# Kernel tuning notes

Hardware: AMD Instinct MI355X
Metric: run time of the kernel (lower is better)

The kernel has to match this reference:

```python
import math
import jax, jax.numpy as jnp
import numpy as np

B, T, C, HS = 4, 4096, 1024, 64  # batch, seq, n_embd, head_size=n_embd//n_head

def setup_inputs() -> dict:
    key = jax.random.key(0)
    k0, k1, k2, k3 = jax.random.split(key, 4)
    x = jax.random.normal(k0, (B, T, C), dtype=jnp.float32)
    Wq = jax.random.normal(k1, (C, HS), dtype=jnp.float32) * 0.02
    Wk = jax.random.normal(k2, (C, HS), dtype=jnp.float32) * 0.02
    Wv = jax.random.normal(k3, (C, HS), dtype=jnp.float32) * 0.02
    return {"x": x, "Wq": Wq, "Wk": Wk, "Wv": Wv}

def reference(x, Wq, Wk, Wv):
    b, t, c = x.shape
    q = x @ Wq                                   # [B,T,hs]
    k = x @ Wk                                   # [B,T,hs]
    v = x @ Wv                                   # [B,T,hs]
    wei = jnp.einsum('btd,bsd->bts', q, k)       # [B,T,T] raw scores
    row_sums = wei.sum(axis=-1)                  # [B,T]
    k_sel = math.ceil(t / 2)                     # static: t known at trace time
    _, idx = jax.lax.top_k(row_sums, k_sel)      # [B,k_sel]
    idx = jnp.sort(idx, axis=1)
    # gather selected score rows: [B,k_sel,T]
    half_wei = jnp.take_along_axis(wei, idx[:, :, None], axis=1)
    # causal mask rows gathered from tril: tril[idx[b,i], j] == (j <= idx[b,i])
    half_mask = jnp.arange(t)[None, None, :] <= idx[:, :, None]  # [B,k_sel,T] bool
    half_wei = half_wei * (c ** -0.5)            # NOTE: scaled by n_embd, as in source
    half_wei = jnp.where(half_mask, half_wei, -jnp.inf)
    att = jax.nn.softmax(half_wei, axis=-1)      # [B,k_sel,T]
    out = att @ v                                # [B,k_sel,hs]
    return out
```

## Files before the change

kernel.cpp:

```cpp
#include <hip/hip_runtime.h>
#include <math.h>

#define BB 4
#define TT 4096
#define CC 1024
#define HS 64
#define KSEL 2048
#define NSPL 16
#define SWLOG 8
#define SW 256

typedef float f32x4 __attribute__((ext_vector_type(4)));
typedef short short8 __attribute__((ext_vector_type(8)));

__device__ __forceinline__ unsigned short f2bf(float f) {
  union { float f; unsigned int u; } c;
  c.f = f;
  const unsigned int u = c.u;
  return (unsigned short)((u + 0x7FFFu + ((u >> 16) & 1u)) >> 16);
}

__device__ __forceinline__ unsigned cvtpk(float lo, float hi) {
  unsigned r;
  asm("v_cvt_pk_bf16_f32 %0, %1, %2" : "=v"(r) : "v"(lo), "v"(hi));
  return r;
}

__global__ __launch_bounds__(256) void conv_w(const float* __restrict__ Wq,
                                              const float* __restrict__ Wk,
                                              const float* __restrict__ Wv,
                                              unsigned short* __restrict__ wbf,
                                              float* __restrict__ xsum) {
  const int gid = blockIdx.x * 256 + threadIdx.x;
  if (gid < 1024)
    ((float4*)xsum)[gid] = make_float4(0.f, 0.f, 0.f, 0.f);
  const int kt = gid / 768;
  const int rem = gid - kt * 768;
  const int nt = rem >> 6, lane = rem & 63;
  const int col = nt * 16 + (lane & 15);
  const float* W = (col < 64) ? Wq : ((col < 128) ? Wk : Wv);
  const int cl = col & 63;
  const int k0 = kt * 32 + (lane >> 4) * 8;
  unsigned short tmp[8];
#pragma unroll
  for (int i = 0; i < 8; i++) tmp[i] = f2bf(W[(size_t)(k0 + i) * HS + cl]);
  uint4 o;
  o.x = tmp[0] | ((unsigned)tmp[1] << 16);
  o.y = tmp[2] | ((unsigned)tmp[3] << 16);
  o.z = tmp[4] | ((unsigned)tmp[5] << 16);
  o.w = tmp[6] | ((unsigned)tmp[7] << 16);
  *(uint4*)(wbf + (size_t)gid * 8) = o;
}

#define PR 16
__global__ __launch_bounds__(256) void fusedproj(
    const float* __restrict__ x, const unsigned short* __restrict__ wbf,
    float* __restrict__ xsum, unsigned short* __restrict__ qbf,
    unsigned short* __restrict__ kbf, unsigned short* __restrict__ vtbf) {
  __shared__ unsigned short Xs[2][PR][256];
  __shared__ float xsred[2][4][256];
  const int rb = blockIdx.x;
  const size_t r0 = (size_t)rb * PR;
  const int tid = threadIdx.x;
  const int wid = tid >> 6, lane = tid & 63;
  const int lhi = lane >> 4, llo = lane & 15;
  const int cl = tid & 63, rg = tid >> 6;
  const int bidx = rb >> 8;

  f32x4 acc[3];
#pragma unroll
  for (int n = 0; n < 3; n++) acc[n] = (f32x4){0.f, 0.f, 0.f, 0.f};

  float4 pf[4];
#pragma unroll
  for (int rr = 0; rr < 4; rr++)
    pf[rr] = *(const float4*)(x + (r0 + rg * 4 + rr) * CC + cl * 4);

  {
    float ps0 = 0.f, ps1 = 0.f, ps2 = 0.f, ps3 = 0.f;
#pragma unroll
    for (int rr = 0; rr < 4; rr++) {
      const int row = rg * 4 + rr;
      float4 v = pf[rr];
      ps0 += v.x; ps1 += v.y; ps2 += v.z; ps3 += v.w;
      *(uint2*)((char*)&Xs[0][0][0] + row * 512 +
                ((((cl >> 1) ^ (row & 7))) << 4) + ((cl & 1) << 3)) =
          make_uint2(cvtpk(v.x, v.y), cvtpk(v.z, v.w));
    }
    xsred[0][rg][cl * 4 + 0] = ps0;
    xsred[0][rg][cl * 4 + 1] = ps1;
    xsred[0][rg][cl * 4 + 2] = ps2;
    xsred[0][rg][cl * 4 + 3] = ps3;
  }
  __syncthreads();

  for (int ch = 0; ch < 4; ch++) {
    const int cur = ch & 1;
    if (ch < 3) {
#pragma unroll
      for (int rr = 0; rr < 4; rr++)
        pf[rr] = *(const float4*)(x + (r0 + rg * 4 + rr) * CC +
                                  (ch + 1) * 256 + cl * 4);
    }
    atomicAdd(&xsum[bidx * CC + ch * 256 + tid],
              xsred[cur][0][tid] + xsred[cur][1][tid] + xsred[cur][2][tid] +
                  xsred[cur][3][tid]);
#pragma unroll
    for (int ktl = 0; ktl < 8; ktl++) {
      short8 af = *(const short8*)((const char*)&Xs[cur][0][0] + llo * 512 +
                                   ((((ktl << 2) + lhi) ^ (llo & 7)) << 4));
      const unsigned short* bp =
          wbf + (((size_t)(ch * 8 + ktl) * 12 + wid * 3) * 64 + lane) * 8;
#pragma unroll
      for (int n = 0; n < 3; n++) {
        short8 bf = *(const short8*)(bp + n * 64 * 8);
        acc[n] = __builtin_amdgcn_mfma_f32_16x16x32_bf16(af, bf, acc[n], 0, 0, 0);
      }
    }
    if (ch < 3) {
      float ps0 = 0.f, ps1 = 0.f, ps2 = 0.f, ps3 = 0.f;
#pragma unroll
      for (int rr = 0; rr < 4; rr++) {
        const int row = rg * 4 + rr;
        float4 v = pf[rr];
        ps0 += v.x; ps1 += v.y; ps2 += v.z; ps3 += v.w;
        *(uint2*)((char*)&Xs[cur ^ 1][0][0] + row * 512 +
                  ((((cl >> 1) ^ (row & 7))) << 4) + ((cl & 1) << 3)) =
            make_uint2(cvtpk(v.x, v.y), cvtpk(v.z, v.w));
      }
      xsred[cur ^ 1][rg][cl * 4 + 0] = ps0;
      xsred[cur ^ 1][rg][cl * 4 + 1] = ps1;
      xsred[cur ^ 1][rg][cl * 4 + 2] = ps2;
      xsred[cur ^ 1][rg][cl * 4 + 3] = ps3;
      __syncthreads();
    }
  }
  const int rbg = (int)r0 + lhi * 4;
#pragma unroll
  for (int n = 0; n < 3; n++) {
    const int col = (wid * 3 + n) * 16 + llo;
    const int mat = col >> 6, cl2 = col & 63;
    if (mat == 0) {
#pragma unroll
      for (int r = 0; r < 4; r++)
        qbf[(size_t)(rbg + r) * HS + cl2] = f2bf(acc[n][r] * 0.03125f);
    } else if (mat == 1) {
#pragma unroll
      for (int r = 0; r < 4; r++)
        kbf[(size_t)(rbg + r) * HS + cl2] = f2bf(acc[n][r]);
    } else {
      const int bb = rbg >> 12, tloc = rbg & (TT - 1);
      *(uint2*)(vtbf + ((size_t)bb * HS + cl2) * TT + tloc) =
          make_uint2(cvtpk(acc[n][0], acc[n][1]), cvtpk(acc[n][2], acc[n][3]));
    }
  }
}

__global__ __launch_bounds__(512) void rowsums_x(
    const float* __restrict__ x, const float* __restrict__ Wq,
    const float* __restrict__ Wk, const float* __restrict__ xsum,
    float* __restrict__ rs) {
  __shared__ float xsl[CC];
  __shared__ float kred[8][HS];
  __shared__ float ksl[HS];
  __shared__ float wl[CC];
  const int g = blockIdx.x;
  const int tid = threadIdx.x;
  const int b = g >> 6;
  *(float2*)(xsl + tid * 2) = *(const float2*)(xsum + b * CC + tid * 2);
  __syncthreads();
  {
    const int g8 = tid >> 6, d = tid & 63;
    const float* wkp = Wk + (size_t)(g8 * 128) * HS + d;
    float s = 0.f;
    for (int c = 0; c < 128; c++) s += xsl[g8 * 128 + c] * wkp[(size_t)c * HS];
    kred[g8][d] = s;
  }
  __syncthreads();
  if (tid < 64) {
    float s = 0.f;
#pragma unroll
    for (int g8 = 0; g8 < 8; g8++) s += kred[g8][tid];
    ksl[tid] = s;
  }
  __syncthreads();
#pragma unroll
  for (int p = 0; p < 2; p++) {
    const int c = tid * 2 + p;
    const float* wqp = Wq + (size_t)c * HS;
    float s = 0.f;
#pragma unroll
    for (int d4 = 0; d4 < 16; d4++) {
      float4 a = *(const float4*)(wqp + d4 * 4);
      float4 kk = *(const float4*)(ksl + d4 * 4);
      s += a.x * kk.x + a.y * kk.y + a.z * kk.z + a.w * kk.w;
    }
    wl[c] = s;
  }
  __syncthreads();
  const size_t row = (size_t)g * 64 + (tid >> 3);
  const int qu = tid & 7;
  const float* xr = x + row * CC + qu * 128;
  const float* wr = wl + qu * 128;
  float s = 0.f;
  for (int e = 0; e < 32; e++) {
    float4 v = *(const float4*)(xr + e * 4);
    float4 w4 = *(const float4*)(wr + e * 4);
    s += v.x * w4.x + v.y * w4.y + v.z * w4.z + v.w * w4.w;
  }
  s += __shfl_xor(s, 1);
  s += __shfl_xor(s, 2);
  s += __shfl_xor(s, 4);
  if (qu == 0) rs[row] = s;
}

__global__ __launch_bounds__(256) void rankk(const float* __restrict__ rs,
                                             int* __restrict__ flag) {
  __shared__ float rl[TT];
  const int g = blockIdx.x;
  const int b = g >> 7, chunk = g & 127;
  const int tid = threadIdx.x;
  const float* rsb = rs + (size_t)b * TT;
  for (int e = tid; e < TT / 4; e += 256)
    *(float4*)(rl + e * 4) = *(const float4*)(rsb + e * 4);
  __syncthreads();
  const int cand = tid >> 3, qu = tid & 7;
  const int t = chunk * 32 + cand;
  const float my = rl[t];
  int cnt = 0;
  for (int e = 0; e < 128; e++) {
    const int s = qu * 512 + e * 4;
    float4 v = *(const float4*)(rl + s);
    cnt += (v.x > my) || (v.x == my && (s + 0) < t);
    cnt += (v.y > my) || (v.y == my && (s + 1) < t);
    cnt += (v.z > my) || (v.z == my && (s + 2) < t);
    cnt += (v.w > my) || (v.w == my && (s + 3) < t);
  }
  cnt += __shfl_xor(cnt, 1);
  cnt += __shfl_xor(cnt, 2);
  cnt += __shfl_xor(cnt, 4);
  if (qu == 0) flag[(size_t)b * TT + t] = (cnt < KSEL) ? 1 : 0;
}

__global__ __launch_bounds__(256) void compact(const int* __restrict__ flag,
                                               int* __restrict__ idx) {
  __shared__ int wsum[4];
  __shared__ int woff[4];
  const int b = blockIdx.x;
  const int tid = threadIdx.x;
  const int wid = tid >> 6, lane = tid & 63;
  const int* fb = flag + (size_t)b * TT;
  const int base = tid * 16;
  int f[16];
  int cnt = 0;
#pragma unroll
  for (int e4 = 0; e4 < 4; e4++) {
    int4 v = *(const int4*)(fb + base + e4 * 4);
    f[e4 * 4 + 0] = v.x; f[e4 * 4 + 1] = v.y;
    f[e4 * 4 + 2] = v.z; f[e4 * 4 + 3] = v.w;
    cnt += v.x + v.y + v.z + v.w;
  }
  int sc = cnt;
#pragma unroll
  for (int d = 1; d < 64; d <<= 1) {
    int v = __shfl_up(sc, d);
    if (lane >= d) sc += v;
  }
  if (lane == 63) wsum[wid] = sc;
  __syncthreads();
  if (tid == 0) {
    int a = 0;
#pragma unroll
    for (int w = 0; w < 4; w++) { woff[w] = a; a += wsum[w]; }
  }
  __syncthreads();
  int pos = woff[wid] + sc - cnt;
#pragma unroll
  for (int e = 0; e < 16; e++)
    if (f[e]) idx[(size_t)b * KSEL + (pos++)] = base + e;
}

struct KF { short8 a0, a1, b0, b1; };
struct VF { short8 v0, v1, v2, v3; };

__global__ __launch_bounds__(256) void attn_mfma(
    const unsigned short* __restrict__ qbf,
    const unsigned short* __restrict__ kbf,
    const unsigned short* __restrict__ vtbf, const int* __restrict__ idx,
    float* __restrict__ pl, float* __restrict__ pacc) {
  __shared__ unsigned short P_lds[4][32][40];
  const int rb = blockIdx.x;
  const int zz = blockIdx.y;
  const int b = blockIdx.z;
  const int tid = threadIdx.x;
  const int wid = tid >> 6, lane = tid & 63;
  const int s = zz * 4 + wid;
  const size_t rbase = (size_t)b * KSEL + rb * 32;
  const int tmaxblk = idx[rbase + 31];
  const int jlo = s << SWLOG;
  if (jlo > tmaxblk) return;

  const int lhi = lane >> 4, llo = lane & 15;
  const int trow0 = idx[rbase + llo];
  const int trow1 = idx[rbase + 16 + llo];
  short8 qf[2][2];
  {
    const unsigned short* qp0 = qbf + ((size_t)b * TT + trow0) * HS + lhi * 8;
    const unsigned short* qp1 = qbf + ((size_t)b * TT + trow1) * HS + lhi * 8;
    qf[0][0] = *(const short8*)(qp0);
    qf[0][1] = *(const short8*)(qp0 + 32);
    qf[1][0] = *(const short8*)(qp1);
    qf[1][1] = *(const short8*)(qp1 + 32);
  }
  f32x4 o[2][4];
#pragma unroll
  for (int mtt = 0; mtt < 2; mtt++)
#pragma unroll
    for (int n = 0; n < 4; n++) o[mtt][n] = (f32x4){0.f, 0.f, 0.f, 0.f};
  float lsum[2] = {0.f, 0.f};

  const unsigned short* kb = kbf + (size_t)b * TT * HS;
  const unsigned short* vb = vtbf + (size_t)b * HS * TT;
  const int jend = min(tmaxblk + 1, jlo + SW);

  auto loadK = [&](int j0) {
    KF K;
    const unsigned short* kp = kb + (size_t)(j0 + llo) * HS + lhi * 8;
    K.a0 = *(const short8*)(kp);
    K.a1 = *(const short8*)(kp + 32);
    K.b0 = *(const short8*)(kp + 16 * HS);
    K.b1 = *(const short8*)(kp + 16 * HS + 32);
    return K;
  };
  auto loadV = [&](int j0) {
    VF V;
    const unsigned short* vp = vb + (size_t)llo * TT + j0 + lhi * 8;
    V.v0 = *(const short8*)(vp);
    V.v1 = *(const short8*)(vp + 16 * TT);
    V.v2 = *(const short8*)(vp + 32 * TT);
    V.v3 = *(const short8*)(vp + 48 * TT);
    return V;
  };

  auto body = [&](int j0, const KF& K, const VF& V) {
    f32x4 sc[2][2];
#pragma unroll
    for (int mtt = 0; mtt < 2; mtt++) {
      f32x4 a = (f32x4){0.f, 0.f, 0.f, 0.f};
      a = __builtin_amdgcn_mfma_f32_16x16x32_bf16(K.a0, qf[mtt][0], a, 0, 0, 0);
      a = __builtin_amdgcn_mfma_f32_16x16x32_bf16(K.a1, qf[mtt][1], a, 0, 0, 0);
      sc[mtt][0] = a;
      f32x4 c = (f32x4){0.f, 0.f, 0.f, 0.f};
      c = __builtin_amdgcn_mfma_f32_16x16x32_bf16(K.b0, qf[mtt][0], c, 0, 0, 0);
      c = __builtin_amdgcn_mfma_f32_16x16x32_bf16(K.b1, qf[mtt][1], c, 0, 0, 0);
      sc[mtt][1] = c;
    }
#pragma unroll
    for (int mtt = 0; mtt < 2; mtt++) {
      const int tr = (mtt == 0) ? trow0 : trow1;
      float p[8];
#pragma unroll
      for (int kt = 0; kt < 2; kt++)
#pragma unroll
        for (int r = 0; r < 4; r++) {
          const int kk = j0 + kt * 16 + lhi * 4 + r;
          const float e = __expf(sc[mtt][kt][r]);
          p[kt * 4 + r] = (kk <= tr) ? e : 0.f;
        }
      lsum[mtt] += ((p[0] + p[1]) + (p[2] + p[3])) +
                   ((p[4] + p[5]) + (p[6] + p[7]));
      *(uint2*)&P_lds[wid][mtt * 16 + llo][lhi * 4] =
          make_uint2(cvtpk(p[0], p[1]), cvtpk(p[2], p[3]));
      *(uint2*)&P_lds[wid][mtt * 16 + llo][16 + lhi * 4] =
          make_uint2(cvtpk(p[4], p[5]), cvtpk(p[6], p[7]));
    }
    short8 pa0 = *(const short8*)&P_lds[wid][llo][lhi * 8];
    short8 pa1 = *(const short8*)&P_lds[wid][16 + llo][lhi * 8];
    o[0][0] = __builtin_amdgcn_mfma_f32_16x16x32_bf16(pa0, V.v0, o[0][0], 0, 0, 0);
    o[1][0] = __builtin_amdgcn_mfma_f32_16x16x32_bf16(pa1, V.v0, o[1][0], 0, 0, 0);
    o[0][1] = __builtin_amdgcn_mfma_f32_16x16x32_bf16(pa0, V.v1, o[0][1], 0, 0, 0);
    o[1][1] = __builtin_amdgcn_mfma_f32_16x16x32_bf16(pa1, V.v1, o[1][1], 0, 0, 0);
    o[0][2] = __builtin_amdgcn_mfma_f32_16x16x32_bf16(pa0, V.v2, o[0][2], 0, 0, 0);
    o[1][2] = __builtin_amdgcn_mfma_f32_16x16x32_bf16(pa1, V.v2, o[1][2], 0, 0, 0);
    o[0][3] = __builtin_amdgcn_mfma_f32_16x16x32_bf16(pa0, V.v3, o[0][3], 0, 0, 0);
    o[1][3] = __builtin_amdgcn_mfma_f32_16x16x32_bf16(pa1, V.v3, o[1][3], 0, 0, 0);
  };

  int j0 = jlo;
  KF ka = loadK(j0), kb2;
  VF va = loadV(j0), vb2;
  for (;;) {
    if (j0 + 32 < jend) { kb2 = loadK(j0 + 32); vb2 = loadV(j0 + 32); }
    body(j0, ka, va);
    j0 += 32;
    if (j0 >= jend) break;
    if (j0 + 32 < jend) { ka = loadK(j0 + 32); va = loadV(j0 + 32); }
    body(j0, kb2, vb2);
    j0 += 32;
    if (j0 >= jend) break;
  }

  lsum[0] += __shfl_xor(lsum[0], 16);
  lsum[0] += __shfl_xor(lsum[0], 32);
  lsum[1] += __shfl_xor(lsum[1], 16);
  lsum[1] += __shfl_xor(lsum[1], 32);
  if (lane < 16) {
    pl[(rbase + llo) * NSPL + s] = lsum[0];
    pl[(rbase + 16 + llo) * NSPL + s] = lsum[1];
  }
#pragma unroll
  for (int mtt = 0; mtt < 2; mtt++)
#pragma unroll
    for (int r = 0; r < 4; r++) {
      const size_t rowi = rbase + mtt * 16 + lhi * 4 + r;
#pragma unroll
      for (int n = 0; n < 4; n++)
        pacc[(rowi * NSPL + s) * HS + n * 16 + llo] = o[mtt][n][r];
    }
}

__global__ __launch_bounds__(256) void attn_combine(
    const float* __restrict__ pl, const float* __restrict__ pacc,
    const int* __restrict__ idx, float* __restrict__ out) {
  const int b = blockIdx.x;
  const int i0 = blockIdx.y * 32;
  const int tid = threadIdx.x;
  const int r = tid >> 3, dg = tid & 7;
  const size_t rowi = (size_t)b * KSEL + i0 + r;
  const int t_r = idx[rowi];
  const int ns = (t_r >> SWLOG) + 1;
  float L = 0.f;
  float o[8] = {0.f, 0.f, 0.f, 0.f, 0.f, 0.f, 0.f, 0.f};
  for (int s = 0; s < ns; s++) {
    L += pl[rowi * NSPL + s];
    const float* pa = pacc + (rowi * NSPL + s) * HS + dg * 8;
    float4 a0 = *(const float4*)(pa);
    float4 a1 = *(const float4*)(pa + 4);
    o[0] += a0.x; o[1] += a0.y; o[2] += a0.z; o[3] += a0.w;
    o[4] += a1.x; o[5] += a1.y; o[6] += a1.z; o[7] += a1.w;
  }
  const float invl = 1.0f / L;
  float* op = out + rowi * HS + dg * 8;
  *(float4*)(op) = make_float4(o[0] * invl, o[1] * invl, o[2] * invl, o[3] * invl);
  *(float4*)(op + 4) = make_float4(o[4] * invl, o[5] * invl, o[6] * invl, o[7] * invl);
}

extern "C" void kernel_launch(void* const* d_in, const int* in_sizes, int n_in,
                              void* d_out, int out_size, void* d_ws,
                              size_t ws_size, hipStream_t stream) {
  const float* x = (const float*)d_in[0];
  const float* Wq = (const float*)d_in[1];
  const float* Wk = (const float*)d_in[2];
  const float* Wv = (const float*)d_in[3];
  float* out = (float*)d_out;

  float* wsf = (float*)d_ws;
  float* pacc = wsf;
  float* xsum = wsf;
  float* rs = xsum + 4096;
  int* flag = (int*)(rs + 16384);
  unsigned short* wbf = (unsigned short*)(flag + 16384);
  unsigned short* qbf = (unsigned short*)(pacc + 8388608);
  unsigned short* kbf = qbf + 1048576;
  unsigned short* vtbf = kbf + 1048576;
  int* idxp = (int*)(vtbf + 1048576);
  float* pl = (float*)(idxp + 8192);

  conv_w<<<96, 256, 0, stream>>>(Wq, Wk, Wv, wbf, xsum);
  fusedproj<<<1024, 256, 0, stream>>>(x, wbf, xsum, qbf, kbf, vtbf);
  rowsums_x<<<256, 512, 0, stream>>>(x, Wq, Wk, xsum, rs);
  rankk<<<512, 256, 0, stream>>>(rs, flag);
  compact<<<BB, 256, 0, stream>>>(flag, idxp);
  attn_mfma<<<dim3(64, 4, BB), 256, 0, stream>>>(qbf, kbf, vtbf, idxp, pl, pacc);
  attn_combine<<<dim3(BB, 64), 256, 0, stream>>>(pl, pacc, idxp, out);
}
```

Measured before the change: 136.0 us.

## Fuse all stages into one cooperative persistent kernel with grid syncs

Replaces the seven-kernel pipeline with a single cooperative kernel of 256 blocks that runs weight conversion, projection, row sums, ranking, compaction, split attention and combine, separated by grid.sync barriers. Work is remapped so each persistent block loops over several tiles per stage, and the projection tile grows to 32 rows with six accumulators per wave. The goal is to remove the launch gaps between kernels. The cost is that only 256 blocks run, which lowers parallelism and occupancy in the heavy projection and attention stages, and each barrier adds grid-wide sync latency. The previous multi-kernel path is kept as a fallback if the cooperative launch fails, and the fallback projection drops its LDS double buffering.

```diff
diff --git a/kernel.cpp b/kernel.cpp
--- a/kernel.cpp
+++ b/kernel.cpp
@@ -1,5 +1,8 @@
 #include <hip/hip_runtime.h>
+#include <hip/hip_cooperative_groups.h>
 #include <math.h>
+
+namespace cg = cooperative_groups;
 
 #define BB 4
 #define TT 4096
@@ -9,6 +12,7 @@
 #define NSPL 16
 #define SWLOG 8
 #define SW 256
+#define NBLK 256
 
 typedef float f32x4 __attribute__((ext_vector_type(4)));
 typedef short short8 __attribute__((ext_vector_type(8)));
@@ -26,14 +30,415 @@
   return r;
 }
 
-__global__ __launch_bounds__(256) void conv_w(const float* __restrict__ Wq,
-                                              const float* __restrict__ Wk,
-                                              const float* __restrict__ Wv,
-                                              unsigned short* __restrict__ wbf,
-                                              float* __restrict__ xsum) {
+__global__ __launch_bounds__(256) void mega(
+    const float* __restrict__ x, const float* __restrict__ Wq,
+    const float* __restrict__ Wk, const float* __restrict__ Wv,
+    float* __restrict__ out, float* __restrict__ xsum, float* __restrict__ rs,
+    int* __restrict__ flag, unsigned short* __restrict__ wbf,
+    unsigned short* __restrict__ qbf, unsigned short* __restrict__ kbf,
+    unsigned short* __restrict__ vtbf, int* __restrict__ idxp,
+    float* __restrict__ pl, float* __restrict__ pacc) {
+  __shared__ __align__(16) unsigned char SM[20480];
+  cg::grid_group grid = cg::this_grid();
+  const int blk = blockIdx.x;
+  const int tid = threadIdx.x;
+  const int wid = tid >> 6, lane = tid & 63;
+  const int lhi = lane >> 4, llo = lane & 15;
+
+  {
+    const int gid = blk * 256 + tid;
+    if (gid < 1024) ((float4*)xsum)[gid] = make_float4(0.f, 0.f, 0.f, 0.f);
+    if (gid < 24576) {
+      const int kt = gid / 768;
+      const int rem = gid - kt * 768;
+      const int nt = rem >> 6, ln = rem & 63;
+      const int col = nt * 16 + (ln & 15);
+      const float* W = (col < 64) ? Wq : ((col < 128) ? Wk : Wv);
+      const int cl = col & 63;
+      const int k0 = kt * 32 + (ln >> 4) * 8;
+      unsigned short tmp[8];
+#pragma unroll
+      for (int i = 0; i < 8; i++) tmp[i] = f2bf(W[(size_t)(k0 + i) * HS + cl]);
+      uint4 o;
+      o.x = tmp[0] | ((unsigned)tmp[1] << 16);
+      o.y = tmp[2] | ((unsigned)tmp[3] << 16);
+      o.z = tmp[4] | ((unsigned)tmp[5] << 16);
+      o.w = tmp[6] | ((unsigned)tmp[7] << 16);
+      *(uint4*)(wbf + (size_t)gid * 8) = o;
+    }
+  }
+  __threadfence();
+  grid.sync();
+
+  {
+    unsigned short* Xs = (unsigned short*)SM;
+    float* xsred = (float*)(SM + 16384);
+    const int cl = tid & 63, rg = tid >> 6;
+    const int mt = wid >> 1, nh = wid & 1;
+#pragma unroll 1
+    for (int it = 0; it < 2; ++it) {
+      const int rblk = blk * 2 + it;
+      const size_t r0 = (size_t)rblk * 32;
+      const int bidx = rblk >> 7;
+      f32x4 acc[6];
+#pragma unroll
+      for (int n = 0; n < 6; n++) acc[n] = (f32x4){0.f, 0.f, 0.f, 0.f};
+      float4 pf[8];
+#pragma unroll
+      for (int rr = 0; rr < 8; rr++)
+        pf[rr] = *(const float4*)(x + (r0 + rg * 8 + rr) * CC + cl * 4);
+
+      for (int ch = 0; ch < 4; ch++) {
+        float ps0 = 0.f, ps1 = 0.f, ps2 = 0.f, ps3 = 0.f;
+#pragma unroll
+        for (int rr = 0; rr < 8; rr++) {
+          const int row = rg * 8 + rr;
+          float4 v = pf[rr];
+          ps0 += v.x; ps1 += v.y; ps2 += v.z; ps3 += v.w;
+          *(uint2*)((char*)Xs + row * 512 + ((((cl >> 1) ^ (row & 7))) << 4) +
+                    ((cl & 1) << 3)) =
+              make_uint2(cvtpk(v.x, v.y), cvtpk(v.z, v.w));
+        }
+        xsred[rg * 256 + cl * 4 + 0] = ps0;
+        xsred[rg * 256 + cl * 4 + 1] = ps1;
+        xsred[rg * 256 + cl * 4 + 2] = ps2;
+        xsred[rg * 256 + cl * 4 + 3] = ps3;
+        __syncthreads();
+        if (ch < 3) {
+#pragma unroll
+          for (int rr = 0; rr < 8; rr++)
+            pf[rr] = *(const float4*)(x + (r0 + rg * 8 + rr) * CC +
+                                      (ch + 1) * 256 + cl * 4);
+        }
+        atomicAdd(&xsum[bidx * CC + ch * 256 + tid],
+                  xsred[tid] + xsred[256 + tid] + xsred[512 + tid] +
+                      xsred[768 + tid]);
+        const int row = mt * 16 + llo;
+#pragma unroll
+        for (int ktl = 0; ktl < 8; ktl++) {
+          short8 af =
+              *(const short8*)((const char*)Xs + row * 512 +
+                               ((((ktl << 2) + lhi) ^ (row & 7)) << 4));
+          const unsigned short* bp =
+              wbf + (((size_t)(ch * 8 + ktl) * 12 + nh * 6) * 64 + lane) * 8;
+#pragma unroll
+          for (int n = 0; n < 6; n++) {
+            short8 bf = *(const short8*)(bp + n * 64 * 8);
+            acc[n] = __builtin_amdgcn_mfma_f32_16x16x32_bf16(af, bf, acc[n],
+                                                             0, 0, 0);
+          }
+        }
+        __syncthreads();
+      }
+      const int rbg = (int)r0 + mt * 16 + lhi * 4;
+#pragma unroll
+      for (int n = 0; n < 6; n++) {
+        const int col = (nh * 6 + n) * 16 + llo;
+        const int mat = col >> 6, cl2 = col & 63;
+        if (mat == 0) {
+#pragma unroll
+          for (int r = 0; r < 4; r++)
+            qbf[(size_t)(rbg + r) * HS + cl2] = f2bf(acc[n][r] * 0.03125f);
+        } else if (mat == 1) {
+#pragma unroll
+          for (int r = 0; r < 4; r++)
+            kbf[(size_t)(rbg + r) * HS + cl2] = f2bf(acc[n][r]);
+        } else {
+          const int bb = rbg >> 12, tloc = rbg & (TT - 1);
+          *(uint2*)(vtbf + ((size_t)bb * HS + cl2) * TT + tloc) = make_uint2(
+              cvtpk(acc[n][0], acc[n][1]), cvtpk(acc[n][2], acc[n][3]));
+        }
+      }
+      __syncthreads();
+    }
+  }
+  __threadfence();
+  grid.sync();
+
+  {
+    float* xsl = (float*)SM;
+    float* kred = xsl + 1024;
+    float* ksl = kred + 256;
+    float* wl = ksl + 64;
+    const int g0 = blk * 2;
+    const int b = g0 >> 7;
+    *(float4*)(xsl + tid * 4) = *(const float4*)(xsum + b * CC + tid * 4);
+    __syncthreads();
+    {
+      float s = 0.f;
+      const float* wkp = Wk + (size_t)(wid * 256) * HS + lane;
+      for (int c = 0; c < 256; c++)
+        s += xsl[wid * 256 + c] * wkp[(size_t)c * HS];
+      kred[wid * 64 + lane] = s;
+    }
+    __syncthreads();
+    if (tid < 64)
+      ksl[tid] = kred[tid] + kred[64 + tid] + kred[128 + tid] + kred[192 + tid];
+    __syncthreads();
+#pragma unroll
+    for (int p = 0; p < 4; p++) {
+      const int c = p * 256 + tid;
+      const float* wqp = Wq + (size_t)c * HS;
+      float s = 0.f;
+#pragma unroll
+      for (int d4 = 0; d4 < 16; d4++) {
+        float4 a = *(const float4*)(wqp + d4 * 4);
+        float4 kk = *(const float4*)(ksl + d4 * 4);
+        s += a.x * kk.x + a.y * kk.y + a.z * kk.z + a.w * kk.w;
+      }
+      wl[c] = s;
+    }
+    __syncthreads();
+#pragma unroll 1
+    for (int it = 0; it < 2; ++it) {
+      const size_t row = (size_t)(g0 + it) * 32 + (tid >> 3);
+      const int qu = tid & 7;
+      const float* xr = x + row * CC + qu * 128;
+      const float* wr = wl + qu * 128;
+      float s = 0.f;
+      for (int e = 0; e < 32; e++) {
+        float4 v = *(const float4*)(xr + e * 4);
+        float4 w4 = *(const float4*)(wr + e * 4);
+        s += v.x * w4.x + v.y * w4.y + v.z * w4.z + v.w * w4.w;
+      }
+      s += __shfl_xor(s, 1);
+      s += __shfl_xor(s, 2);
+      s += __shfl_xor(s, 4);
+      if (qu == 0) rs[row] = s;
+    }
+  }
+  __threadfence();
+  grid.sync();
+
+  {
+    float* rl = (float*)SM;
+    const int g0 = blk * 2;
+    const int b = g0 >> 7;
+    const float* rsb = rs + (size_t)b * TT;
+    for (int e = tid; e < TT / 4; e += 256)
+      *(float4*)(rl + e * 4) = *(const float4*)(rsb + e * 4);
+    __syncthreads();
+#pragma unroll 1
+    for (int it = 0; it < 2; ++it) {
+      const int chunk = (g0 + it) & 127;
+      const int cand = tid >> 3, qu = tid & 7;
+      const int t = chunk * 32 + cand;
+      const float my = rl[t];
+      int cnt = 0;
+      for (int e = 0; e < 128; e++) {
+        const int s = qu * 512 + e * 4;
+        float4 v = *(const float4*)(rl + s);
+        cnt += (v.x > my) || (v.x == my && (s + 0) < t);
+        cnt += (v.y > my) || (v.y == my && (s + 1) < t);
+        cnt += (v.z > my) || (v.z == my && (s + 2) < t);
+        cnt += (v.w > my) || (v.w == my && (s + 3) < t);
+      }
+      cnt += __shfl_xor(cnt, 1);
+      cnt += __shfl_xor(cnt, 2);
+      cnt += __shfl_xor(cnt, 4);
+      if (qu == 0) flag[(size_t)b * TT + t] = (cnt < KSEL) ? 1 : 0;
+    }
+  }
+  __threadfence();
+  grid.sync();
+
+  if (blk < BB) {
+    int* wsum = (int*)SM;
+    int* woff = wsum + 4;
+    const int* fb = flag + (size_t)blk * TT;
+    const int base = tid * 16;
+    int f[16];
+    int cnt = 0;
+#pragma unroll
+    for (int e4 = 0; e4 < 4; e4++) {
+      int4 v = *(const int4*)(fb + base + e4 * 4);
+      f[e4 * 4 + 0] = v.x; f[e4 * 4 + 1] = v.y;
+      f[e4 * 4 + 2] = v.z; f[e4 * 4 + 3] = v.w;
+      cnt += v.x + v.y + v.z + v.w;
+    }
+    int sc = cnt;
+#pragma unroll
+    for (int d = 1; d < 64; d <<= 1) {
+      int v = __shfl_up(sc, d);
+      if (lane >= d) sc += v;
+    }
+    if (lane == 63) wsum[wid] = sc;
+    __syncthreads();
+    if (tid == 0) {
+      int a = 0;
+#pragma unroll
+      for (int w = 0; w < 4; w++) { woff[w] = a; a += wsum[w]; }
+    }
+    __syncthreads();
+    int pos = woff[wid] + sc - cnt;
+#pragma unroll
+    for (int e = 0; e < 16; e++)
+      if (f[e]) idxp[(size_t)blk * KSEL + (pos++)] = base + e;
+  }
+  __threadfence();
+  grid.sync();
+
+  {
+    unsigned short* P = (unsigned short*)SM;
+    unsigned short* Pw = P + wid * 32 * 40;
+#pragma unroll 1
+    for (int half = 0; half < 4; half++) {
+      const int u = (blk * 4 + wid) + half * 1024;
+      const int b = u & 3;
+      const int rb = (u >> 2) & 63;
+      const int sp = u >> 8;
+      const size_t rbase = (size_t)b * KSEL + rb * 32;
+      const int tmaxblk = idxp[rbase + 31];
+      const int jlo = sp << SWLOG;
+      if (jlo > tmaxblk) continue;
+
+      const int trow0 = idxp[rbase + llo];
+      const int trow1 = idxp[rbase + 16 + llo];
+      short8 qf[2][2];
+      {
+        const unsigned short* qp0 =
+            qbf + ((size_t)b * TT + trow0) * HS + lhi * 8;
+        const unsigned short* qp1 =
+            qbf + ((size_t)b * TT + trow1) * HS + lhi * 8;
+        qf[0][0] = *(const short8*)(qp0);
+        qf[0][1] = *(const short8*)(qp0 + 32);
+        qf[1][0] = *(const short8*)(qp1);
+        qf[1][1] = *(const short8*)(qp1 + 32);
+      }
+      f32x4 o[2][4];
+#pragma unroll
+      for (int mtt = 0; mtt < 2; mtt++)
+#pragma unroll
+        for (int n = 0; n < 4; n++) o[mtt][n] = (f32x4){0.f, 0.f, 0.f, 0.f};
+      float lsum[2] = {0.f, 0.f};
+
+      const unsigned short* kb = kbf + (size_t)b * TT * HS;
+      const unsigned short* vb = vtbf + (size_t)b * HS * TT;
+      const int jend = min(tmaxblk + 1, jlo + SW);
+
+      auto loadK = [&](int j0, short8* K) {
+        const unsigned short* kp = kb + (size_t)(j0 + llo) * HS + lhi * 8;
+        K[0] = *(const short8*)(kp);
+        K[1] = *(const short8*)(kp + 32);
+        K[2] = *(const short8*)(kp + 16 * HS);
+        K[3] = *(const short8*)(kp + 16 * HS + 32);
+      };
+      auto loadV = [&](int j0, short8* V) {
+        const unsigned short* vp = vb + (size_t)llo * TT + j0 + lhi * 8;
+        V[0] = *(const short8*)(vp);
+        V[1] = *(const short8*)(vp + 16 * TT);
+        V[2] = *(const short8*)(vp + 32 * TT);
+        V[3] = *(const short8*)(vp + 48 * TT);
+      };
+
+      auto body = [&](int j0, const short8* K, const short8* V) {
+        f32x4 sc[2][2];
+#pragma unroll
+        for (int mtt = 0; mtt < 2; mtt++) {
+          f32x4 a = (f32x4){0.f, 0.f, 0.f, 0.f};
+          a = __builtin_amdgcn_mfma_f32_16x16x32_bf16(K[0], qf[mtt][0], a, 0, 0, 0);
+          a = __builtin_amdgcn_mfma_f32_16x16x32_bf16(K[1], qf[mtt][1], a, 0, 0, 0);
+          sc[mtt][0] = a;
+          f32x4 c = (f32x4){0.f, 0.f, 0.f, 0.f};
+          c = __builtin_amdgcn_mfma_f32_16x16x32_bf16(K[2], qf[mtt][0], c, 0, 0, 0);
+          c = __builtin_amdgcn_mfma_f32_16x16x32_bf16(K[3], qf[mtt][1], c, 0, 0, 0);
+          sc[mtt][1] = c;
+        }
+#pragma unroll
+        for (int mtt = 0; mtt < 2; mtt++) {
+          const int tr = (mtt == 0) ? trow0 : trow1;
+          float p[8];
+#pragma unroll
+          for (int kt = 0; kt < 2; kt++)
+#pragma unroll
+            for (int r = 0; r < 4; r++) {
+              const int kk = j0 + kt * 16 + lhi * 4 + r;
+              const float e = __expf(sc[mtt][kt][r]);
+              p[kt * 4 + r] = (kk <= tr) ? e : 0.f;
+            }
+          lsum[mtt] += ((p[0] + p[1]) + (p[2] + p[3])) +
+                       ((p[4] + p[5]) + (p[6] + p[7]));
+          *(uint2*)&Pw[(mtt * 16 + llo) * 40 + lhi * 4] =
+              make_uint2(cvtpk(p[0], p[1]), cvtpk(p[2], p[3]));
+          *(uint2*)&Pw[(mtt * 16 + llo) * 40 + 16 + lhi * 4] =
+              make_uint2(cvtpk(p[4], p[5]), cvtpk(p[6], p[7]));
+        }
+        short8 pa0 = *(const short8*)&Pw[llo * 40 + lhi * 8];
+        short8 pa1 = *(const short8*)&Pw[(16 + llo) * 40 + lhi * 8];
+        o[0][0] = __builtin_amdgcn_mfma_f32_16x16x32_bf16(pa0, V[0], o[0][0], 0, 0, 0);
+        o[1][0] = __builtin_amdgcn_mfma_f32_16x16x32_bf16(pa1, V[0], o[1][0], 0, 0, 0);
+        o[0][1] = __builtin_amdgcn_mfma_f32_16x16x32_bf16(pa0, V[1], o[0][1], 0, 0, 0);
+        o[1][1] = __builtin_amdgcn_mfma_f32_16x16x32_bf16(pa1, V[1], o[1][1], 0, 0, 0);
+        o[0][2] = __builtin_amdgcn_mfma_f32_16x16x32_bf16(pa0, V[2], o[0][2], 0, 0, 0);
+        o[1][2] = __builtin_amdgcn_mfma_f32_16x16x32_bf16(pa1, V[2], o[1][2], 0, 0, 0);
+        o[0][3] = __builtin_amdgcn_mfma_f32_16x16x32_bf16(pa0, V[3], o[0][3], 0, 0, 0);
+        o[1][3] = __builtin_amdgcn_mfma_f32_16x16x32_bf16(pa1, V[3], o[1][3], 0, 0, 0);
+      };
+
+      int j0 = jlo;
+      short8 ka[4], kb2[4], va[4], vb2[4];
+      loadK(j0, ka);
+      loadV(j0, va);
+      for (;;) {
+        if (j0 + 32 < jend) { loadK(j0 + 32, kb2); loadV(j0 + 32, vb2); }
+        body(j0, ka, va);
+        j0 += 32;
+        if (j0 >= jend) break;
+        if (j0 + 32 < jend) { loadK(j0 + 32, ka); loadV(j0 + 32, va); }
+        body(j0, kb2, vb2);
+        j0 += 32;
+        if (j0 >= jend) break;
+      }
+
+      lsum[0] += __shfl_xor(lsum[0], 16);
+      lsum[0] += __shfl_xor(lsum[0], 32);
+      lsum[1] += __shfl_xor(lsum[1], 16);
+      lsum[1] += __shfl_xor(lsum[1], 32);
+      if (lane < 16) {
+        pl[(rbase + llo) * NSPL + sp] = lsum[0];
+        pl[(rbase + 16 + llo) * NSPL + sp] = lsum[1];
+      }
+#pragma unroll
+      for (int mtt = 0; mtt < 2; mtt++)
+#pragma unroll
+        for (int r = 0; r < 4; r++) {
+          const size_t rowi = rbase + mtt * 16 + lhi * 4 + r;
+#pragma unroll
+          for (int n = 0; n < 4; n++)
+            pacc[(rowi * NSPL + sp) * HS + n * 16 + llo] = o[mtt][n][r];
+        }
+    }
+  }
+  __threadfence();
+  grid.sync();
+
+  {
+#pragma unroll 1
+    for (int it = 0; it < 2; ++it) {
+      const int r = tid >> 4, dg = tid & 15;
+      const size_t rowi = (size_t)(blk * 2 + it) * 16 + r;
+      const int t_r = idxp[rowi];
+      const int ns = (t_r >> SWLOG) + 1;
+      float L = 0.f;
+      float o0 = 0.f, o1 = 0.f, o2 = 0.f, o3 = 0.f;
+      for (int s = 0; s < ns; s++) {
+        L += pl[rowi * NSPL + s];
+        float4 a = *(const float4*)(pacc + (rowi * NSPL + s) * HS + dg * 4);
+        o0 += a.x; o1 += a.y; o2 += a.z; o3 += a.w;
+      }
+      const float invl = 1.0f / L;
+      *(float4*)(out + rowi * HS + dg * 4) =
+          make_float4(o0 * invl, o1 * invl, o2 * invl, o3 * invl);
+    }
+  }
+}
+
+__global__ __launch_bounds__(256) void conv_w_fb(
+    const float* __restrict__ Wq, const float* __restrict__ Wk,
+    const float* __restrict__ Wv, unsigned short* __restrict__ wbf,
+    float* __restrict__ xsum) {
   const int gid = blockIdx.x * 256 + threadIdx.x;
-  if (gid < 1024)
-    ((float4*)xsum)[gid] = make_float4(0.f, 0.f, 0.f, 0.f);
+  if (gid < 1024) ((float4*)xsum)[gid] = make_float4(0.f, 0.f, 0.f, 0.f);
   const int kt = gid / 768;
   const int rem = gid - kt * 768;
   const int nt = rem >> 6, lane = rem & 63;
@@ -52,50 +457,42 @@
   *(uint4*)(wbf + (size_t)gid * 8) = o;
 }
 
-#define PR 16
-__global__ __launch_bounds__(256) void fusedproj(
+__global__ __launch_bounds__(256) void fusedproj_fb(
     const float* __restrict__ x, const unsigned short* __restrict__ wbf,
     float* __restrict__ xsum, unsigned short* __restrict__ qbf,
     unsigned short* __restrict__ kbf, unsigned short* __restrict__ vtbf) {
-  __shared__ unsigned short Xs[2][PR][256];
-  __shared__ float xsred[2][4][256];
+  __shared__ unsigned short Xs[16][256];
+  __shared__ float xsred[4][256];
   const int rb = blockIdx.x;
-  const size_t r0 = (size_t)rb * PR;
+  const size_t r0 = (size_t)rb * 16;
   const int tid = threadIdx.x;
   const int wid = tid >> 6, lane = tid & 63;
   const int lhi = lane >> 4, llo = lane & 15;
   const int cl = tid & 63, rg = tid >> 6;
   const int bidx = rb >> 8;
-
   f32x4 acc[3];
 #pragma unroll
   for (int n = 0; n < 3; n++) acc[n] = (f32x4){0.f, 0.f, 0.f, 0.f};
-
   float4 pf[4];
 #pragma unroll
   for (int rr = 0; rr < 4; rr++)
     pf[rr] = *(const float4*)(x + (r0 + rg * 4 + rr) * CC + cl * 4);
-
-  {
+  for (int ch = 0; ch < 4; ch++) {
     float ps0 = 0.f, ps1 = 0.f, ps2 = 0.f, ps3 = 0.f;
 #pragma unroll
     for (int rr = 0; rr < 4; rr++) {
       const int row = rg * 4 + rr;
       float4 v = pf[rr];
       ps0 += v.x; ps1 += v.y; ps2 += v.z; ps3 += v.w;
-      *(uint2*)((char*)&Xs[0][0][0] + row * 512 +
+      *(uint2*)((char*)&Xs[0][0] + row * 512 +
                 ((((cl >> 1) ^ (row & 7))) << 4) + ((cl & 1) << 3)) =
           make_uint2(cvtpk(v.x, v.y), cvtpk(v.z, v.w));
     }
-    xsred[0][rg][cl * 4 + 0] = ps0;
-    xsred[0][rg][cl * 4 + 1] = ps1;
-    xsred[0][rg][cl * 4 + 2] = ps2;
-    xsred[0][rg][cl * 4 + 3] = ps3;
-  }
-  __syncthreads();
-
-  for (int ch = 0; ch < 4; ch++) {
-    const int cur = ch & 1;
+    xsred[rg][cl * 4 + 0] = ps0;
+    xsred[rg][cl * 4 + 1] = ps1;
+    xsred[rg][cl * 4 + 2] = ps2;
+    xsred[rg][cl * 4 + 3] = ps3;
+    __syncthreads();
     if (ch < 3) {
 #pragma unroll
       for (int rr = 0; rr < 4; rr++)
@@ -103,11 +500,10 @@
                                   (ch + 1) * 256 + cl * 4);
     }
     atomicAdd(&xsum[bidx * CC + ch * 256 + tid],
-              xsred[cur][0][tid] + xsred[cur][1][tid] + xsred[cur][2][tid] +
-                  xsred[cur][3][tid]);
+              xsred[0][tid] + xsred[1][tid] + xsred[2][tid] + xsred[3][tid]);
 #pragma unroll
     for (int ktl = 0; ktl < 8; ktl++) {
-      short8 af = *(const short8*)((const char*)&Xs[cur][0][0] + llo * 512 +
+      short8 af = *(const short8*)((const char*)&Xs[0][0] + llo * 512 +
                                    ((((ktl << 2) + lhi) ^ (llo & 7)) << 4));
       const unsigned short* bp =
           wbf + (((size_t)(ch * 8 + ktl) * 12 + wid * 3) * 64 + lane) * 8;
@@ -117,23 +513,7 @@
         acc[n] = __builtin_amdgcn_mfma_f32_16x16x32_bf16(af, bf, acc[n], 0, 0, 0);
       }
     }
-    if (ch < 3) {
-      float ps0 = 0.f, ps1 = 0.f, ps2 = 0.f, ps3 = 0.f;
-#pragma unroll
-      for (int rr = 0; rr < 4; rr++) {
-        const int row = rg * 4 + rr;
-        float4 v = pf[rr];
-        ps0 += v.x; ps1 += v.y; ps2 += v.z; ps3 += v.w;
-        *(uint2*)((char*)&Xs[cur ^ 1][0][0] + row * 512 +
-                  ((((cl >> 1) ^ (row & 7))) << 4) + ((cl & 1) << 3)) =
-            make_uint2(cvtpk(v.x, v.y), cvtpk(v.z, v.w));
-      }
-      xsred[cur ^ 1][rg][cl * 4 + 0] = ps0;
-      xsred[cur ^ 1][rg][cl * 4 + 1] = ps1;
-      xsred[cur ^ 1][rg][cl * 4 + 2] = ps2;
-      xsred[cur ^ 1][rg][cl * 4 + 3] = ps3;
-      __syncthreads();
-    }
+    __syncthreads();
   }
   const int rbg = (int)r0 + lhi * 4;
 #pragma unroll
@@ -156,7 +536,7 @@
   }
 }
 
-__global__ __launch_bounds__(512) void rowsums_x(
+__global__ __launch_bounds__(512) void rowsums_fb(
     const float* __restrict__ x, const float* __restrict__ Wq,
     const float* __restrict__ Wk, const float* __restrict__ xsum,
     float* __restrict__ rs) {
@@ -214,8 +594,8 @@
   if (qu == 0) rs[row] = s;
 }
 
-__global__ __launch_bounds__(256) void rankk(const float* __restrict__ rs,
-                                             int* __restrict__ flag) {
+__global__ __launch_bounds__(256) void rankk_fb(const float* __restrict__ rs,
+                                                int* __restrict__ flag) {
   __shared__ float rl[TT];
   const int g = blockIdx.x;
   const int b = g >> 7, chunk = g & 127;
@@ -242,8 +622,8 @@
   if (qu == 0) flag[(size_t)b * TT + t] = (cnt < KSEL) ? 1 : 0;
 }
 
-__global__ __launch_bounds__(256) void compact(const int* __restrict__ flag,
-                                               int* __restrict__ idx) {
+__global__ __launch_bounds__(256) void compact_fb(const int* __restrict__ flag,
+                                                  int* __restrict__ idx) {
   __shared__ int wsum[4];
   __shared__ int woff[4];
   const int b = blockIdx.x;
@@ -280,10 +660,7 @@
     if (f[e]) idx[(size_t)b * KSEL + (pos++)] = base + e;
 }
 
-struct KF { short8 a0, a1, b0, b1; };
-struct VF { short8 v0, v1, v2, v3; };
-
-__global__ __launch_bounds__(256) void attn_mfma(
+__global__ __launch_bounds__(256) void attn_fb(
     const unsigned short* __restrict__ qbf,
     const unsigned short* __restrict__ kbf,
     const unsigned short* __restrict__ vtbf, const int* __restrict__ idx,
@@ -299,7 +676,6 @@
   const int tmaxblk = idx[rbase + 31];
   const int jlo = s << SWLOG;
   if (jlo > tmaxblk) return;
-
   const int lhi = lane >> 4, llo = lane & 15;
   const int trow0 = idx[rbase + llo];
   const int trow1 = idx[rbase + 16 + llo];
@@ -318,41 +694,34 @@
 #pragma unroll
     for (int n = 0; n < 4; n++) o[mtt][n] = (f32x4){0.f, 0.f, 0.f, 0.f};
   float lsum[2] = {0.f, 0.f};
-
   const unsigned short* kb = kbf + (size_t)b * TT * HS;
   const unsigned short* vb = vtbf + (size_t)b * HS * TT;
   const int jend = min(tmaxblk + 1, jlo + SW);
-
-  auto loadK = [&](int j0) {
-    KF K;
+  auto loadK = [&](int j0, short8* K) {
     const unsigned short* kp = kb + (size_t)(j0 + llo) * HS + lhi * 8;
-    K.a0 = *(const short8*)(kp);
-    K.a1 = *(const short8*)(kp + 32);
-    K.b0 = *(const short8*)(kp + 16 * HS);
-    K.b1 = *(const short8*)(kp + 16 * HS + 32);
-    return K;
+    K[0] = *(const short8*)(kp);
+    K[1] = *(const short8*)(kp + 32);
+    K[2] = *(const short8*)(kp + 16 * HS);
+    K[3] = *(const short8*)(kp + 16 * HS + 32);
   };
-  auto loadV = [&](int j0) {
-    VF V;
+  auto loadV = [&](int j0, short8* V) {
     const unsigned short* vp = vb + (size_t)llo * TT + j0 + lhi * 8;
-    V.v0 = *(const short8*)(vp);
-    V.v1 = *(const short8*)(vp + 16 * TT);
-    V.v2 = *(const short8*)(vp + 32 * TT);
-    V.v3 = *(const short8*)(vp + 48 * TT);
-    return V;
+    V[0] = *(const short8*)(vp);
+    V[1] = *(const short8*)(vp + 16 * TT);
+    V[2] = *(const short8*)(vp + 32 * TT);
+    V[3] = *(const short8*)(vp + 48 * TT);
   };
-
-  auto body = [&](int j0, const KF& K, const VF& V) {
+  auto body = [&](int j0, const short8* K, const short8* V) {
     f32x4 sc[2][2];
 #pragma unroll
     for (int mtt = 0; mtt < 2; mtt++) {
       f32x4 a = (f32x4){0.f, 0.f, 0.f, 0.f};
-      a = __builtin_amdgcn_mfma_f32_16x16x32_bf16(K.a0, qf[mtt][0], a, 0, 0, 0);
-      a = __builtin_amdgcn_mfma_f32_16x16x32_bf16(K.a1, qf[mtt][1], a, 0, 0, 0);
+      a = __builtin_amdgcn_mfma_f32_16x16x32_bf16(K[0], qf[mtt][0], a, 0, 0, 0);
+      a = __builtin_amdgcn_mfma_f32_16x16x32_bf16(K[1], qf[mtt][1], a, 0, 0, 0);
       sc[mtt][0] = a;
       f32x4 c = (f32x4){0.f, 0.f, 0.f, 0.f};
-      c = __builtin_amdgcn_mfma_f32_16x16x32_bf16(K.b0, qf[mtt][0], c, 0, 0, 0);
-      c = __builtin_amdgcn_mfma_f32_16x16x32_bf16(K.b1, qf[mtt][1], c, 0, 0, 0);
+      c = __builtin_amdgcn_mfma_f32_16x16x32_bf16(K[2], qf[mtt][0], c, 0, 0, 0);
+      c = __builtin_amdgcn_mfma_f32_16x16x32_bf16(K[3], qf[mtt][1], c, 0, 0, 0);
       sc[mtt][1] = c;
     }
 #pragma unroll
@@ -376,30 +745,29 @@
     }
     short8 pa0 = *(const short8*)&P_lds[wid][llo][lhi * 8];
     short8 pa1 = *(const short8*)&P_lds[wid][16 + llo][lhi * 8];
-    o[0][0] = __builtin_amdgcn_mfma_f32_16x16x32_bf16(pa0, V.v0, o[0][0], 0, 0, 0);
-    o[1][0] = __builtin_amdgcn_mfma_f32_16x16x32_bf16(pa1, V.v0, o[1][0], 0, 0, 0);
-    o[0][1] = __builtin_amdgcn_mfma_f32_16x16x32_bf16(pa0, V.v1, o[0][1], 0, 0, 0);
-    o[1][1] = __builtin_amdgcn_mfma_f32_16x16x32_bf16(pa1, V.v1, o[1][1], 0, 0, 0);
-    o[0][2] = __builtin_amdgcn_mfma_f32_16x16x32_bf16(pa0, V.v2, o[0][2], 0, 0, 0);
-    o[1][2] = __builtin_amdgcn_mfma_f32_16x16x32_bf16(pa1, V.v2, o[1][2], 0, 0, 0);
-    o[0][3] = __builtin_amdgcn_mfma_f32_16x16x32_bf16(pa0, V.v3, o[0][3], 0, 0, 0);
-    o[1][3] = __builtin_amdgcn_mfma_f32_16x16x32_bf16(pa1, V.v3, o[1][3], 0, 0, 0);
+    o[0][0] = __builtin_amdgcn_mfma_f32_16x16x32_bf16(pa0, V[0], o[0][0], 0, 0, 0);
+    o[1][0] = __builtin_amdgcn_mfma_f32_16x16x32_bf16(pa1, V[0], o[1][0], 0, 0, 0);
+    o[0][1] = __builtin_amdgcn_mfma_f32_16x16x32_bf16(pa0, V[1], o[0][1], 0, 0, 0);
+    o[1][1] = __builtin_amdgcn_mfma_f32_16x16x32_bf16(pa1, V[1], o[1][1], 0, 0, 0);
+    o[0][2] = __builtin_amdgcn_mfma_f32_16x16x32_bf16(pa0, V[2], o[0][2], 0, 0, 0);
+    o[1][2] = __builtin_amdgcn_mfma_f32_16x16x32_bf16(pa1, V[2], o[1][2], 0, 0, 0);
+    o[0][3] = __builtin_amdgcn_mfma_f32_16x16x32_bf16(pa0, V[3], o[0][3], 0, 0, 0);
+    o[1][3] = __builtin_amdgcn_mfma_f32_16x16x32_bf16(pa1, V[3], o[1][3], 0, 0, 0);
   };
-
   int j0 = jlo;
-  KF ka = loadK(j0), kb2;
-  VF va = loadV(j0), vb2;
+  short8 ka[4], kb2[4], va[4], vb2[4];
+  loadK(j0, ka);
+  loadV(j0, va);
   for (;;) {
-    if (j0 + 32 < jend) { kb2 = loadK(j0 + 32); vb2 = loadV(j0 + 32); }
+    if (j0 + 32 < jend) { loadK(j0 + 32, kb2); loadV(j0 + 32, vb2); }
     body(j0, ka, va);
     j0 += 32;
     if (j0 >= jend) break;
-    if (j0 + 32 < jend) { ka = loadK(j0 + 32); va = loadV(j0 + 32); }
+    if (j0 + 32 < jend) { loadK(j0 + 32, ka); loadV(j0 + 32, va); }
     body(j0, kb2, vb2);
     j0 += 32;
     if (j0 >= jend) break;
   }
-
   lsum[0] += __shfl_xor(lsum[0], 16);
   lsum[0] += __shfl_xor(lsum[0], 32);
   lsum[1] += __shfl_xor(lsum[1], 16);
@@ -419,7 +787,7 @@
     }
 }
 
-__global__ __launch_bounds__(256) void attn_combine(
+__global__ __launch_bounds__(256) void combine_fb(
     const float* __restrict__ pl, const float* __restrict__ pacc,
     const int* __restrict__ idx, float* __restrict__ out) {
   const int b = blockIdx.x;
@@ -466,11 +834,20 @@
   int* idxp = (int*)(vtbf + 1048576);
   float* pl = (float*)(idxp + 8192);
 
-  conv_w<<<96, 256, 0, stream>>>(Wq, Wk, Wv, wbf, xsum);
-  fusedproj<<<1024, 256, 0, stream>>>(x, wbf, xsum, qbf, kbf, vtbf);
-  rowsums_x<<<256, 512, 0, stream>>>(x, Wq, Wk, xsum, rs);
-  rankk<<<512, 256, 0, stream>>>(rs, flag);
-  compact<<<BB, 256, 0, stream>>>(flag, idxp);
-  attn_mfma<<<dim3(64, 4, BB), 256, 0, stream>>>(qbf, kbf, vtbf, idxp, pl, pacc);
-  attn_combine<<<dim3(BB, 64), 256, 0, stream>>>(pl, pacc, idxp, out);
-}
+  void* args[] = {(void*)&x,    (void*)&Wq,   (void*)&Wk,   (void*)&Wv,
+                  (void*)&out,  (void*)&xsum, (void*)&rs,   (void*)&flag,
+                  (void*)&wbf,  (void*)&qbf,  (void*)&kbf,  (void*)&vtbf,
+                  (void*)&idxp, (void*)&pl,   (void*)&pacc};
+  hipError_t err = hipLaunchCooperativeKernel((const void*)mega, dim3(NBLK),
+                                              dim3(256), args, 0, stream);
+  if (err != hipSuccess) {
+    (void)hipGetLastError();
+    conv_w_fb<<<96, 256, 0, stream>>>(Wq, Wk, Wv, wbf, xsum);
+    fusedproj_fb<<<1024, 256, 0, stream>>>(x, wbf, xsum, qbf, kbf, vtbf);
+    rowsums_fb<<<256, 512, 0, stream>>>(x, Wq, Wk, xsum, rs);
+    rankk_fb<<<512, 256, 0, stream>>>(rs, flag);
+    compact_fb<<<BB, 256, 0, stream>>>(flag, idxp);
+    attn_fb<<<dim3(64, 4, BB), 256, 0, stream>>>(qbf, kbf, vtbf, idxp, pl, pacc);
+    combine_fb<<<dim3(BB, 64), 256, 0, stream>>>(pl, pacc, idxp, out);
+  }
+}
```

New measurement: 538.5 us. +296.0%, slower.
